# Kernel tuning notes

Hardware: AMD Instinct MI355X
Metric: run time of the kernel (lower is better)

## Reference

```python
import jax, jax.numpy as jnp
import numpy as np

B, N, D, R, H, E = 4, 8192, 16, 32, 64, 262144


def _linear_init(key, fan_in, fan_out):
    return jax.random.normal(key, (fan_in, fan_out), jnp.float32) * (1.0 / np.sqrt(fan_in))


def setup_inputs() -> dict:
    key = jax.random.key(0)
    ks = jax.random.split(key, 8)
    particles = jax.random.normal(ks[0], (B, N, D), jnp.float32)
    senders = jax.random.randint(ks[1], (E,), 0, N, dtype=jnp.int32)
    receivers = jax.random.randint(ks[2], (E,), 0, N, dtype=jnp.int32)
    # relation_encoder: Linear(2D->H), ReLU, Linear(H->R), ReLU
    W1 = _linear_init(ks[3], 2 * D, H)
    b1 = jnp.zeros((H,), jnp.float32)
    W2 = _linear_init(ks[4], H, R)
    b2 = jnp.zeros((R,), jnp.float32)
    # dynamics_fn: Linear(D+R->H), ReLU, Linear(H->D)
    W3 = _linear_init(ks[5], D + R, H)
    b3 = jnp.zeros((H,), jnp.float32)
    W4 = _linear_init(ks[6], H, D)
    b4 = jnp.zeros((D,), jnp.float32)
    return {"particles": particles, "senders": senders, "receivers": receivers,
            "W1": W1, "b1": b1, "W2": W2, "b2": b2,
            "W3": W3, "b3": b3, "W4": W4, "b4": b4}


def reference(particles, senders, receivers, W1, b1, W2, b2, W3, b3, W4, b4):
    # Gather per-edge sender/receiver states: [B, E, D]
    send = particles[:, senders, :]
    recv = particles[:, receivers, :]
    edge_in = jnp.concatenate([send, recv], axis=-1)          # [B, E, 2D]
    # relation_encoder (one batched GEMM over all edges)
    h = jax.nn.relu(edge_in @ W1 + b1)                        # [B, E, H]
    rel_feat = jax.nn.relu(h @ W2 + b2)                       # [B, E, R]
    # scatter-add edge features into receiver nodes
    Bp, Np, _ = particles.shape
    rel = jnp.zeros((Bp, Np, rel_feat.shape[-1]), particles.dtype)
    rel = rel.at[:, receivers, :].add(rel_feat)               # [B, N, R]
    # node update MLP
    dyn_in = jnp.concatenate([particles, rel], axis=-1)       # [B, N, D+R]
    delta = jax.nn.relu(dyn_in @ W3 + b3) @ W4 + b4           # [B, N, D]
    return particles + delta
```

## Files before the change

### kernel.cpp

```cpp
#include <hip/hip_runtime.h>
#include <hip/hip_bf16.h>

namespace {

constexpr int B = 4;
constexpr int N = 8192;
constexpr int D = 16;
constexpr int R = 32;
constexpr int H = 64;
constexpr int E = 262144;

typedef __attribute__((ext_vector_type(8))) short short8;
typedef __attribute__((ext_vector_type(4))) short short4v;
typedef __attribute__((ext_vector_type(4))) float f32x4;

__device__ __forceinline__ float4 ld4(const float* p) {
    return *reinterpret_cast<const float4*>(p);
}
__device__ __forceinline__ float4 fma4(float a, float4 w, float4 c) {
    return float4{fmaf(a, w.x, c.x), fmaf(a, w.y, c.y),
                  fmaf(a, w.z, c.z), fmaf(a, w.w, c.w)};
}
__device__ __forceinline__ float4 relu4(float4 v) {
    return float4{fmaxf(v.x, 0.f), fmaxf(v.y, 0.f), fmaxf(v.z, 0.f), fmaxf(v.w, 0.f)};
}
__device__ __forceinline__ short bf16s(float f) {
    __hip_bfloat16 h = __float2bfloat16(f);
    return __builtin_bit_cast(short, h);
}
__device__ __forceinline__ short8 pack8(float4 a, float4 b) {
    short8 o;
    o[0] = bf16s(a.x); o[1] = bf16s(a.y); o[2] = bf16s(a.z); o[3] = bf16s(a.w);
    o[4] = bf16s(b.x); o[5] = bf16s(b.y); o[6] = bf16s(b.z); o[7] = bf16s(b.w);
    return o;
}
__device__ __forceinline__ short4v pack4_relu(f32x4 c) {
    short4v o;
    o[0] = bf16s(fmaxf(c[0], 0.f)); o[1] = bf16s(fmaxf(c[1], 0.f));
    o[2] = bf16s(fmaxf(c[2], 0.f)); o[3] = bf16s(fmaxf(c[3], 0.f));
    return o;
}
__device__ __forceinline__ float red_get(const int4* uu, int i) {
    const int wsel = i >> 1;
    const int4 v = uu[wsel >> 2];
    const int word = (wsel & 3) == 0 ? v.x : (wsel & 3) == 1 ? v.y
                   : (wsel & 3) == 2 ? v.z : v.w;
    return (i & 1) ? __builtin_bit_cast(float, word & 0xffff0000)
                   : __builtin_bit_cast(float, (unsigned)word << 16);
}

constexpr int RED_S = 264;

__device__ __forceinline__ void prepack_w12(
    int t, const float* __restrict__ W1, const float* __restrict__ W2,
    short* __restrict__ w1p, short* __restrict__ w2p)
{
    for (int i = t; i < 4 * 64 * 8; i += 256) {
        int j = i & 7, lane = (i >> 3) & 63, ct = i >> 9;
        int k = (lane >> 4) * 8 + j, n = ct * 16 + (lane & 15);
        w1p[i] = bf16s(W1[k * H + n]);
    }
    for (int i = t; i < 4 * 64 * 8; i += 256) {
        int j = i & 7, lane = (i >> 3) & 63, idx = i >> 9;
        int ct = idx >> 1, kc = idx & 1;
        int k = kc * 32 + (lane >> 4) * 8 + j, f = ct * 16 + (lane & 15);
        w2p[i] = bf16s(W2[k * R + f]);
    }
}
__device__ __forceinline__ void prepack_w34(
    int t, const float* __restrict__ W3, const float* __restrict__ W4,
    short* __restrict__ w3p, short* __restrict__ w4p)
{
    for (int i = t; i < 8 * 64 * 8; i += 256) {
        int j = i & 7, lane = (i >> 3) & 63, idx = i >> 9;
        int ct = idx >> 1, kc = idx & 1;
        int k = kc * 32 + (lane >> 4) * 8 + j, n = ct * 16 + (lane & 15);
        w3p[i] = (k < D + R) ? bf16s(W3[k * H + n]) : (short)0;
    }
    for (int i = t; i < 2 * 64 * 8; i += 256) {
        int j = i & 7, lane = (i >> 3) & 63, kc = i >> 9;
        int k = kc * 32 + (lane >> 4) * 8 + j, d = lane & 15;
        w4p[i] = bf16s(W4[k * D + d]);
    }
}


__global__ __launch_bounds__(256) void hist_prepack_kernel(
    const int* __restrict__ receivers, int* __restrict__ cnt,
    const float* __restrict__ W1, const float* __restrict__ W2,
    const float* __restrict__ W3, const float* __restrict__ W4,
    short* __restrict__ w1p, short* __restrict__ w2p,
    short* __restrict__ w3p, short* __restrict__ w4p,
    float4* __restrict__ relz)
{
    if (blockIdx.x < 1024) {
        int e = blockIdx.x * 256 + threadIdx.x;
        atomicAdd(cnt + receivers[e], 1);
        return;
    }
    if (blockIdx.x >= 1025) {
        const int base = (blockIdx.x - 1025) * 256 + threadIdx.x;
        #pragma unroll
        for (int i = 0; i < 8; ++i)
            relz[base + i * 32768] = float4{0.f, 0.f, 0.f, 0.f};
        return;
    }
    prepack_w12(threadIdx.x, W1, W2, w1p, w2p);
    prepack_w34(threadIdx.x, W3, W4, w3p, w4p);
}

__global__ __launch_bounds__(1024) void scan_kernel(
    const int* __restrict__ cnt, int* __restrict__ pos)
{
    __shared__ int wtot[16];
    const int t = threadIdx.x;
    const int lane = t & 63;
    int local[8];
    int s = 0;
    #pragma unroll
    for (int i = 0; i < 8; ++i) { local[i] = cnt[t * 8 + i]; s += local[i]; }
    int incl = s;
    #pragma unroll
    for (int d = 1; d < 64; d <<= 1) {
        int v = __shfl_up(incl, d, 64);
        if (lane >= d) incl += v;
    }
    if (lane == 63) wtot[t >> 6] = incl;
    __syncthreads();
    int base = incl - s;
    const int wv = t >> 6;
    #pragma unroll
    for (int i = 0; i < 16; ++i) base += (i < wv) ? wtot[i] : 0;
    #pragma unroll
    for (int i = 0; i < 8; ++i) {
        pos[t * 8 + i] = base;
        base += local[i];
    }
}

__global__ __launch_bounds__(256) void scatter_kernel(
    const int* __restrict__ senders, const int* __restrict__ receivers,
    int* __restrict__ pos, int2* __restrict__ sr)
{
    int e = blockIdx.x * 256 + threadIdx.x;
    if (e < E) {
        int r = receivers[e];
        int p = atomicAdd(pos + r, 1);
        sr[p] = int2{senders[e], r};
    }
}

__global__ __launch_bounds__(256, 3) void edge_mfma_kernel(
    const float* __restrict__ particles,
    const int2*  __restrict__ sr,
    const short* __restrict__ w1p, const float* __restrict__ b1,
    const short* __restrict__ w2p, const float* __restrict__ b2,
    float* __restrict__ rel)
{
    __shared__ short red[R * RED_S];
    __shared__ short hbuf[4][16 * 72];
    __shared__ int   rs[256];

    const int tid  = threadIdx.x;
    const int lane = tid & 63;
    const int w    = tid >> 6;
    const int p0   = blockIdx.x * 256;
    const int l15  = lane & 15;
    const int q    = lane >> 4;

    const int2 srv = sr[p0 + tid];
    rs[tid] = srv.y;

    int rowoff[4];
    #pragma unroll
    for (int t = 0; t < 4; ++t) {
        int srow = __shfl(srv.x, t * 16 + l15);
        int rrow = __shfl(srv.y, t * 16 + l15);
        rowoff[t] = ((q < 2) ? srow : rrow) * D + (q & 1) * 8;
    }

    short8 w1f[4], w2f[4];
    #pragma unroll
    for (int mt = 0; mt < 4; ++mt)
        w1f[mt] = *reinterpret_cast<const short8*>(w1p + (mt * 64 + lane) * 8);
    #pragma unroll
    for (int i = 0; i < 4; ++i)
        w2f[i] = *reinterpret_cast<const short8*>(w2p + (i * 64 + lane) * 8);

    f32x4 bias1[4];
    #pragma unroll
    for (int mt = 0; mt < 4; ++mt) {
        float4 t4 = ld4(b1 + mt * 16 + q * 4);
        bias1[mt] = f32x4{t4.x, t4.y, t4.z, t4.w};
    }
    const float bias2a = b2[l15];
    const float bias2b = b2[16 + l15];

    float4 ga[4], gb[4];
    #pragma unroll
    for (int t = 0; t < 4; ++t) {
        const float* src = particles + rowoff[t];
        ga[t] = ld4(src);
        gb[t] = ld4(src + 4);
    }

    short* hb = &hbuf[w][0];

    for (int bb = 0; bb < B; ++bb) {
        short8 af[4];
        #pragma unroll
        for (int t = 0; t < 4; ++t) af[t] = pack8(ga[t], gb[t]);

        if (bb + 1 < B) {
            const float* pb = particles + (size_t)(bb + 1) * N * D;
            #pragma unroll
            for (int t = 0; t < 4; ++t) {
                const float* src = pb + rowoff[t];
                ga[t] = ld4(src);
                gb[t] = ld4(src + 4);
            }
        }

        #pragma unroll
        for (int t = 0; t < 4; ++t) {
            #pragma unroll
            for (int mt = 0; mt < 4; ++mt) {
                f32x4 c = bias1[mt];
                c = __builtin_amdgcn_mfma_f32_16x16x32_bf16(w1f[mt], af[t], c, 0, 0, 0);
                *reinterpret_cast<short4v*>(hb + l15 * 72 + mt * 16 + q * 4) = pack4_relu(c);
            }
            short8 h0 = *reinterpret_cast<const short8*>(hb + l15 * 72 + q * 8);
            short8 h1 = *reinterpret_cast<const short8*>(hb + l15 * 72 + 32 + q * 8);

            f32x4 r0 = {bias2a, bias2a, bias2a, bias2a};
            f32x4 r1 = {bias2b, bias2b, bias2b, bias2b};
            r0 = __builtin_amdgcn_mfma_f32_16x16x32_bf16(h0, w2f[0], r0, 0, 0, 0);
            r0 = __builtin_amdgcn_mfma_f32_16x16x32_bf16(h1, w2f[1], r0, 0, 0, 0);
            r1 = __builtin_amdgcn_mfma_f32_16x16x32_bf16(h0, w2f[2], r1, 0, 0, 0);
            r1 = __builtin_amdgcn_mfma_f32_16x16x32_bf16(h1, w2f[3], r1, 0, 0, 0);

            const int pb2 = w * 64 + t * 16 + q * 4;
            *reinterpret_cast<short4v*>(red + l15 * RED_S + pb2)        = pack4_relu(r0);
            *reinterpret_cast<short4v*>(red + (16 + l15) * RED_S + pb2) = pack4_relu(r1);
        }
        __syncthreads();

        {
            const int g = tid >> 5;
            const int f = tid & 31;
            const int base = g * 32;
            float* relb = rel + (size_t)bb * N * R;

            int4 uu[4];
            #pragma unroll
            for (int i = 0; i < 4; ++i)
                uu[i] = *reinterpret_cast<const int4*>(red + f * RED_S + base + 8 * i);
            int4 r4[8];
            #pragma unroll
            for (int i = 0; i < 8; ++i)
                r4[i] = *reinterpret_cast<const int4*>(rs + base + 4 * i);

            const int first = r4[0].x;
            const int last  = r4[7].w;
            if (first == last) {
                float acc = 0.f;
                #pragma unroll
                for (int i = 0; i < 32; ++i) acc += red_get(uu, i);
                atomicAdd(relb + (size_t)first * R + f, acc);
            } else {
                float acc = 0.f;
                int cur = first;
                #pragma unroll
                for (int i = 0; i < 32; ++i) {
                    int rr = (i & 3) == 0 ? r4[i >> 2].x : (i & 3) == 1 ? r4[i >> 2].y
                           : (i & 3) == 2 ? r4[i >> 2].z : r4[i >> 2].w;
                    float v = red_get(uu, i);
                    if (rr != cur) {
                        atomicAdd(relb + (size_t)cur * R + f, acc);
                        acc = 0.f;
                        cur = rr;
                    }
                    acc += v;
                }
                atomicAdd(relb + (size_t)cur * R + f, acc);
            }
        }
        __syncthreads();
    }
}

__global__ __launch_bounds__(256, 4) void node_mfma_kernel(
    const float* __restrict__ particles,
    const float* __restrict__ rel,
    const short* __restrict__ w3p, const float* __restrict__ b3,
    const short* __restrict__ w4p, const float* __restrict__ b4,
    float* __restrict__ out)
{
    __shared__ short hbuf[4][16 * 72];

    const int tid  = threadIdx.x;
    const int lane = tid & 63;
    const int w    = tid >> 6;
    const int tile = blockIdx.x * 4 + w;
    const int b    = tile >> 9;
    const int l15  = lane & 15;
    const int q    = lane >> 4;
    const int node = (tile & 511) * 16 + l15;

    const float* prow = particles + ((size_t)b * N + node) * D;
    const float* rrow = rel + ((size_t)b * N + node) * R;

    const float* src0 = (q < 2) ? (prow + (q & 1) * 8) : (rrow + (q & 1) * 8);
    float4 c0a = ld4(src0), c0b = ld4(src0 + 4);
    float4 c1a = {0.f, 0.f, 0.f, 0.f}, c1b = {0.f, 0.f, 0.f, 0.f};
    if (q < 2) { c1a = ld4(rrow + 16 + q * 8); c1b = ld4(rrow + 20 + q * 8); }

    short8 w3f[8], w4f[2];
    #pragma unroll
    for (int i = 0; i < 8; ++i)
        w3f[i] = *reinterpret_cast<const short8*>(w3p + (i * 64 + lane) * 8);
    #pragma unroll
    for (int i = 0; i < 2; ++i)
        w4f[i] = *reinterpret_cast<const short8*>(w4p + (i * 64 + lane) * 8);

    f32x4 bias3[4];
    #pragma unroll
    for (int mt = 0; mt < 4; ++mt) {
        float4 t4 = ld4(b3 + mt * 16 + q * 4);
        bias3[mt] = f32x4{t4.x, t4.y, t4.z, t4.w};
    }
    f32x4 bias4;
    { float4 t4 = ld4(b4 + q * 4); bias4 = f32x4{t4.x, t4.y, t4.z, t4.w}; }

    short8 a0 = pack8(c0a, c0b);
    short8 a1 = pack8(c1a, c1b);

    short* hb = &hbuf[w][0];
    #pragma unroll
    for (int mt = 0; mt < 4; ++mt) {
        f32x4 c = bias3[mt];
        c = __builtin_amdgcn_mfma_f32_16x16x32_bf16(w3f[mt * 2 + 0], a0, c, 0, 0, 0);
        c = __builtin_amdgcn_mfma_f32_16x16x32_bf16(w3f[mt * 2 + 1], a1, c, 0, 0, 0);
        *reinterpret_cast<short4v*>(hb + l15 * 72 + mt * 16 + q * 4) = pack4_relu(c);
    }
    short8 h0 = *reinterpret_cast<const short8*>(hb + l15 * 72 + q * 8);
    short8 h1 = *reinterpret_cast<const short8*>(hb + l15 * 72 + 32 + q * 8);

    f32x4 r = bias4;
    r = __builtin_amdgcn_mfma_f32_16x16x32_bf16(w4f[0], h0, r, 0, 0, 0);
    r = __builtin_amdgcn_mfma_f32_16x16x32_bf16(w4f[1], h1, r, 0, 0, 0);

    float4 pv = ld4(prow + q * 4);
    float4* po = reinterpret_cast<float4*>(out + ((size_t)b * N + node) * D + q * 4);
    *po = float4{pv.x + r[0], pv.y + r[1], pv.z + r[2], pv.w + r[3]};
}


__global__ __launch_bounds__(256, 2) void edge_atomic_kernel(
    const float* __restrict__ particles,
    const int*   __restrict__ senders,
    const int*   __restrict__ receivers,
    const float* __restrict__ W1, const float* __restrict__ b1,
    const float* __restrict__ W2, const float* __restrict__ b2,
    float* __restrict__ rel)
{
    const int idx = blockIdx.x * 256 + threadIdx.x;
    const int b = idx >> 18;
    const int e = idx & (E - 1);
    const int s = senders[e];
    const int r = receivers[e];

    float4 ein4[8];
    {
        const float4* ps = reinterpret_cast<const float4*>(particles + ((size_t)b * N + s) * D);
        const float4* pr = reinterpret_cast<const float4*>(particles + ((size_t)b * N + r) * D);
        #pragma unroll
        for (int qq = 0; qq < 4; ++qq) ein4[qq] = ps[qq];
        #pragma unroll
        for (int qq = 0; qq < 4; ++qq) ein4[4 + qq] = pr[qq];
    }
    float4 rf4[8];
    #pragma unroll
    for (int qq = 0; qq < 8; ++qq) rf4[qq] = ld4(b2 + 4 * qq);

    for (int j4 = 0; j4 < H / 4; ++j4) {
        float4 h = ld4(b1 + 4 * j4);
        const float* w1c = W1 + 4 * j4;
        #pragma unroll
        for (int kv = 0; kv < 8; ++kv) {
            const float4 ev = ein4[kv];
            h = fma4(ev.x, ld4(w1c + (4 * kv + 0) * H), h);
            h = fma4(ev.y, ld4(w1c + (4 * kv + 1) * H), h);
            h = fma4(ev.z, ld4(w1c + (4 * kv + 2) * H), h);
            h = fma4(ev.w, ld4(w1c + (4 * kv + 3) * H), h);
        }
        h = relu4(h);
        const float* w2r = W2 + (4 * j4) * R;
        #pragma unroll
        for (int qq = 0; qq < 4; ++qq) {
            const float hq = (qq == 0) ? h.x : (qq == 1) ? h.y : (qq == 2) ? h.z : h.w;
            #pragma unroll
            for (int r4 = 0; r4 < 8; ++r4)
                rf4[r4] = fma4(hq, ld4(w2r + qq * R + 4 * r4), rf4[r4]);
        }
    }
    float* dst = rel + ((size_t)b * N + r) * R;
    #pragma unroll
    for (int r4 = 0; r4 < 8; ++r4) {
        float4 v = relu4(rf4[r4]);
        atomicAdd(dst + 4 * r4 + 0, v.x);
        atomicAdd(dst + 4 * r4 + 1, v.y);
        atomicAdd(dst + 4 * r4 + 2, v.z);
        atomicAdd(dst + 4 * r4 + 3, v.w);
    }
}

__global__ __launch_bounds__(256, 2) void node_valu_kernel(
    const float* __restrict__ particles,
    const float* __restrict__ rel,
    const float* __restrict__ W3, const float* __restrict__ b3,
    const float* __restrict__ W4, const float* __restrict__ b4,
    float* __restrict__ out)
{
    const int idx = blockIdx.x * 256 + threadIdx.x;
    float4 in4[12];
    {
        const float4* pp = reinterpret_cast<const float4*>(particles + (size_t)idx * D);
        #pragma unroll
        for (int qq = 0; qq < 4; ++qq) in4[qq] = pp[qq];
        const float4* pr = reinterpret_cast<const float4*>(rel + (size_t)idx * R);
        #pragma unroll
        for (int qq = 0; qq < 8; ++qq) in4[4 + qq] = pr[qq];
    }
    float4 dl4[4];
    #pragma unroll
    for (int qq = 0; qq < 4; ++qq) dl4[qq] = ld4(b4 + 4 * qq);

    for (int j4 = 0; j4 < H / 4; ++j4) {
        float4 h = ld4(b3 + 4 * j4);
        const float* w3c = W3 + 4 * j4;
        #pragma unroll
        for (int kv = 0; kv < 12; ++kv) {
            const float4 ev = in4[kv];
            h = fma4(ev.x, ld4(w3c + (4 * kv + 0) * H), h);
            h = fma4(ev.y, ld4(w3c + (4 * kv + 1) * H), h);
            h = fma4(ev.z, ld4(w3c + (4 * kv + 2) * H), h);
            h = fma4(ev.w, ld4(w3c + (4 * kv + 3) * H), h);
        }
        h = relu4(h);
        const float* w4r = W4 + (4 * j4) * D;
        #pragma unroll
        for (int qq = 0; qq < 4; ++qq) {
            const float hq = (qq == 0) ? h.x : (qq == 1) ? h.y : (qq == 2) ? h.z : h.w;
            #pragma unroll
            for (int d4 = 0; d4 < 4; ++d4)
                dl4[d4] = fma4(hq, ld4(w4r + qq * D + 4 * d4), dl4[d4]);
        }
    }
    float4* po = reinterpret_cast<float4*>(out + (size_t)idx * D);
    #pragma unroll
    for (int qq = 0; qq < 4; ++qq) {
        float4 v = dl4[qq];
        float4 pv = in4[qq];
        po[qq] = float4{pv.x + v.x, pv.y + v.y, pv.z + v.z, pv.w + v.w};
    }
}

}

extern "C" void kernel_launch(void* const* d_in, const int* in_sizes, int n_in,
                              void* d_out, int out_size, void* d_ws, size_t ws_size,
                              hipStream_t stream) {
    const float* particles = (const float*)d_in[0];
    const int*   senders   = (const int*)d_in[1];
    const int*   receivers = (const int*)d_in[2];
    const float* W1 = (const float*)d_in[3];
    const float* b1 = (const float*)d_in[4];
    const float* W2 = (const float*)d_in[5];
    const float* b2 = (const float*)d_in[6];
    const float* W3 = (const float*)d_in[7];
    const float* b3 = (const float*)d_in[8];
    const float* W4 = (const float*)d_in[9];
    const float* b4 = (const float*)d_in[10];
    float* out = (float*)d_out;

    char* ws = (char*)d_ws;
    size_t off = 0;
    auto take = [&](size_t bytes) -> char* {
        char* p = ws + off;
        off = (off + bytes + 255) & ~(size_t)255;
        return p;
    };
    int*   cnt     = (int*)  take((size_t)N * 4);
    int*   pos     = (int*)  take((size_t)N * 4);
    int2*  sr      = (int2*) take((size_t)E * 8);
    float* rel     = (float*)take((size_t)B * N * R * 4);
    short* w1p     = (short*)take((size_t)4 * 64 * 8 * 2);
    short* w2p     = (short*)take((size_t)4 * 64 * 8 * 2);
    short* w3p     = (short*)take((size_t)8 * 64 * 8 * 2);
    short* w4p     = (short*)take((size_t)2 * 64 * 8 * 2);
    const bool fast = (off <= ws_size);

    if (fast) {
        hipMemsetAsync(cnt, 0, (size_t)N * 4, stream);
        hist_prepack_kernel<<<1153, 256, 0, stream>>>(
            receivers, cnt, W1, W2, W3, W4, w1p, w2p, w3p, w4p, (float4*)rel);
        scan_kernel<<<1, 1024, 0, stream>>>(cnt, pos);
        scatter_kernel<<<E / 256, 256, 0, stream>>>(senders, receivers, pos, sr);
        edge_mfma_kernel<<<E / 256, 256, 0, stream>>>(
            particles, sr, w1p, b1, w2p, b2, rel);
        node_mfma_kernel<<<(B * N / 16) / 4, 256, 0, stream>>>(
            particles, rel, w3p, b3, w4p, b4, out);
    } else {
        float* rel0 = (float*)d_ws;
        hipMemsetAsync(rel0, 0, (size_t)B * N * R * 4, stream);
        edge_atomic_kernel<<<(B * E) / 256, 256, 0, stream>>>(
            particles, senders, receivers, W1, b1, W2, b2, rel0);
        node_valu_kernel<<<(B * N) / 256, 256, 0, stream>>>(
            particles, rel0, W3, b3, W4, b4, out);
    }
}
```

Before: 141.8 us.

## Split edge kernel across batches per block and swizzle hidden LDS layout

The edge MFMA kernel now launches one block per (batch, 256-edge chunk) instead of looping over the four batches inside each block. This drops the in-block batch loop, the software prefetch of the next batch and one barrier per batch, and raises the occupancy hint from 3 to 4 blocks. It also rotates the hidden-activation LDS column layout per row to reduce bank conflicts on the h0/h1 reads. In exchange, each block reloads the sender/receiver indices and the weight fragments, giving four times the setup work and index reads.

```diff
diff --git a/kernel.cpp b/kernel.cpp
--- a/kernel.cpp
+++ b/kernel.cpp
@@ -150,7 +150,7 @@
     }
 }
 
-__global__ __launch_bounds__(256, 3) void edge_mfma_kernel(
+__global__ __launch_bounds__(256, 4) void edge_mfma_kernel(
     const float* __restrict__ particles,
     const int2*  __restrict__ sr,
     const short* __restrict__ w1p, const float* __restrict__ b1,
@@ -164,19 +164,23 @@
     const int tid  = threadIdx.x;
     const int lane = tid & 63;
     const int w    = tid >> 6;
-    const int p0   = blockIdx.x * 256;
+    const int b    = blockIdx.x >> 10;
+    const int p0   = (blockIdx.x & 1023) * 256;
     const int l15  = lane & 15;
     const int q    = lane >> 4;
 
     const int2 srv = sr[p0 + tid];
     rs[tid] = srv.y;
 
-    int rowoff[4];
+    float4 a0[4], a1[4];
     #pragma unroll
     for (int t = 0; t < 4; ++t) {
         int srow = __shfl(srv.x, t * 16 + l15);
         int rrow = __shfl(srv.y, t * 16 + l15);
-        rowoff[t] = ((q < 2) ? srow : rrow) * D + (q & 1) * 8;
+        int row = (q < 2) ? srow : rrow;
+        const float* src = particles + ((size_t)b * N + row) * D + (q & 1) * 8;
+        a0[t] = ld4(src);
+        a1[t] = ld4(src + 4);
     }
 
     short8 w1f[4], w2f[4];
@@ -196,96 +200,75 @@
     const float bias2a = b2[l15];
     const float bias2b = b2[16 + l15];
 
-    float4 ga[4], gb[4];
+    short8 af[4];
+    #pragma unroll
+    for (int t = 0; t < 4; ++t) af[t] = pack8(a0[t], a1[t]);
+
+    short* hb = &hbuf[w][0];
+
     #pragma unroll
     for (int t = 0; t < 4; ++t) {
-        const float* src = particles + rowoff[t];
-        ga[t] = ld4(src);
-        gb[t] = ld4(src + 4);
-    }
-
-    short* hb = &hbuf[w][0];
-
-    for (int bb = 0; bb < B; ++bb) {
-        short8 af[4];
-        #pragma unroll
-        for (int t = 0; t < 4; ++t) af[t] = pack8(ga[t], gb[t]);
-
-        if (bb + 1 < B) {
-            const float* pb = particles + (size_t)(bb + 1) * N * D;
-            #pragma unroll
-            for (int t = 0; t < 4; ++t) {
-                const float* src = pb + rowoff[t];
-                ga[t] = ld4(src);
-                gb[t] = ld4(src + 4);
+        #pragma unroll
+        for (int mt = 0; mt < 4; ++mt) {
+            f32x4 c = bias1[mt];
+            c = __builtin_amdgcn_mfma_f32_16x16x32_bf16(w1f[mt], af[t], c, 0, 0, 0);
+            const int smt = (mt + l15) & 3;
+            *reinterpret_cast<short4v*>(hb + l15 * 72 + smt * 16 + q * 4) = pack4_relu(c);
+        }
+        const int sm0 = ((q >> 1) + l15) & 3;
+        const int sm1 = (2 + (q >> 1) + l15) & 3;
+        short8 h0 = *reinterpret_cast<const short8*>(hb + l15 * 72 + sm0 * 16 + (q & 1) * 8);
+        short8 h1 = *reinterpret_cast<const short8*>(hb + l15 * 72 + sm1 * 16 + (q & 1) * 8);
+
+        f32x4 r0 = {bias2a, bias2a, bias2a, bias2a};
+        f32x4 r1 = {bias2b, bias2b, bias2b, bias2b};
+        r0 = __builtin_amdgcn_mfma_f32_16x16x32_bf16(h0, w2f[0], r0, 0, 0, 0);
+        r0 = __builtin_amdgcn_mfma_f32_16x16x32_bf16(h1, w2f[1], r0, 0, 0, 0);
+        r1 = __builtin_amdgcn_mfma_f32_16x16x32_bf16(h0, w2f[2], r1, 0, 0, 0);
+        r1 = __builtin_amdgcn_mfma_f32_16x16x32_bf16(h1, w2f[3], r1, 0, 0, 0);
+
+        const int pb2 = w * 64 + t * 16 + q * 4;
+        *reinterpret_cast<short4v*>(red + l15 * RED_S + pb2)        = pack4_relu(r0);
+        *reinterpret_cast<short4v*>(red + (16 + l15) * RED_S + pb2) = pack4_relu(r1);
+    }
+    __syncthreads();
+
+    const int g = tid >> 5;
+    const int f = tid & 31;
+    const int base = g * 32;
+
+    int4 uu[4];
+    #pragma unroll
+    for (int i = 0; i < 4; ++i)
+        uu[i] = *reinterpret_cast<const int4*>(red + f * RED_S + base + 8 * i);
+    int4 r4[8];
+    #pragma unroll
+    for (int i = 0; i < 8; ++i)
+        r4[i] = *reinterpret_cast<const int4*>(rs + base + 4 * i);
+
+    const int first = r4[0].x;
+    const int last  = r4[7].w;
+    if (first == last) {
+        float acc = 0.f;
+        #pragma unroll
+        for (int i = 0; i < 32; ++i) acc += red_get(uu, i);
+        atomicAdd(rel + ((size_t)b * N + first) * R + f, acc);
+    } else {
+        float acc = 0.f;
+        int cur = first;
+        #pragma unroll
+        for (int i = 0; i < 32; ++i) {
+            int rr = (i & 3) == 0 ? r4[i >> 2].x : (i & 3) == 1 ? r4[i >> 2].y
+                   : (i & 3) == 2 ? r4[i >> 2].z : r4[i >> 2].w;
+            float v = red_get(uu, i);
+            if (rr != cur) {
+                atomicAdd(rel + ((size_t)b * N + cur) * R + f, acc);
+                acc = 0.f;
+                cur = rr;
             }
+            acc += v;
         }
-
-        #pragma unroll
-        for (int t = 0; t < 4; ++t) {
-            #pragma unroll
-            for (int mt = 0; mt < 4; ++mt) {
-                f32x4 c = bias1[mt];
-                c = __builtin_amdgcn_mfma_f32_16x16x32_bf16(w1f[mt], af[t], c, 0, 0, 0);
-                *reinterpret_cast<short4v*>(hb + l15 * 72 + mt * 16 + q * 4) = pack4_relu(c);
-            }
-            short8 h0 = *reinterpret_cast<const short8*>(hb + l15 * 72 + q * 8);
-            short8 h1 = *reinterpret_cast<const short8*>(hb + l15 * 72 + 32 + q * 8);
-
-            f32x4 r0 = {bias2a, bias2a, bias2a, bias2a};
-            f32x4 r1 = {bias2b, bias2b, bias2b, bias2b};
-            r0 = __builtin_amdgcn_mfma_f32_16x16x32_bf16(h0, w2f[0], r0, 0, 0, 0);
-            r0 = __builtin_amdgcn_mfma_f32_16x16x32_bf16(h1, w2f[1], r0, 0, 0, 0);
-            r1 = __builtin_amdgcn_mfma_f32_16x16x32_bf16(h0, w2f[2], r1, 0, 0, 0);
-            r1 = __builtin_amdgcn_mfma_f32_16x16x32_bf16(h1, w2f[3], r1, 0, 0, 0);
-
-            const int pb2 = w * 64 + t * 16 + q * 4;
-            *reinterpret_cast<short4v*>(red + l15 * RED_S + pb2)        = pack4_relu(r0);
-            *reinterpret_cast<short4v*>(red + (16 + l15) * RED_S + pb2) = pack4_relu(r1);
-        }
-        __syncthreads();
-
-        {
-            const int g = tid >> 5;
-            const int f = tid & 31;
-            const int base = g * 32;
-            float* relb = rel + (size_t)bb * N * R;
-
-            int4 uu[4];
-            #pragma unroll
-            for (int i = 0; i < 4; ++i)
-                uu[i] = *reinterpret_cast<const int4*>(red + f * RED_S + base + 8 * i);
-            int4 r4[8];
-            #pragma unroll
-            for (int i = 0; i < 8; ++i)
-                r4[i] = *reinterpret_cast<const int4*>(rs + base + 4 * i);
-
-            const int first = r4[0].x;
-            const int last  = r4[7].w;
-            if (first == last) {
-                float acc = 0.f;
-                #pragma unroll
-                for (int i = 0; i < 32; ++i) acc += red_get(uu, i);
-                atomicAdd(relb + (size_t)first * R + f, acc);
-            } else {
-                float acc = 0.f;
-                int cur = first;
-                #pragma unroll
-                for (int i = 0; i < 32; ++i) {
-                    int rr = (i & 3) == 0 ? r4[i >> 2].x : (i & 3) == 1 ? r4[i >> 2].y
-                           : (i & 3) == 2 ? r4[i >> 2].z : r4[i >> 2].w;
-                    float v = red_get(uu, i);
-                    if (rr != cur) {
-                        atomicAdd(relb + (size_t)cur * R + f, acc);
-                        acc = 0.f;
-                        cur = rr;
-                    }
-                    acc += v;
-                }
-                atomicAdd(relb + (size_t)cur * R + f, acc);
-            }
-        }
-        __syncthreads();
+        atomicAdd(rel + ((size_t)b * N + cur) * R + f, acc);
     }
 }
 
@@ -507,7 +490,7 @@
             receivers, cnt, W1, W2, W3, W4, w1p, w2p, w3p, w4p, (float4*)rel);
         scan_kernel<<<1, 1024, 0, stream>>>(cnt, pos);
         scatter_kernel<<<E / 256, 256, 0, stream>>>(senders, receivers, pos, sr);
-        edge_mfma_kernel<<<E / 256, 256, 0, stream>>>(
+        edge_mfma_kernel<<<(B * E) / 256, 256, 0, stream>>>(
             particles, sr, w1p, b1, w2p, b2, rel);
         node_mfma_kernel<<<(B * N / 16) / 4, 256, 0, stream>>>(
             particles, rel, w3p, b3, w4p, b4, out);
```

New measurement: 137.4 us, median of 2. 1.03x faster.
